# Optimization experiments

Measured on AMD Instinct MI355X. Metric: run time of the kernel, lower is better.

The kernel has to match this reference:

```python
import jax, jax.numpy as jnp
import numpy as np

N_NODES, N_EDGES, F_IN, DIM, N_GRAPHS = 50000, 800000, 128, 256, 256


def setup_inputs() -> dict:
    key = jax.random.key(0)
    ks = jax.random.split(key, 6)
    x = jax.random.normal(ks[0], (N_NODES, F_IN), jnp.float32)
    src = jax.random.randint(ks[1], (N_EDGES,), 0, N_NODES, jnp.int32)
    dst = jax.random.randint(ks[2], (N_EDGES,), 0, N_NODES, jnp.int32)
    node2graph = jnp.sort(jax.random.randint(ks[3], (N_NODES,), 0, N_GRAPHS, jnp.int32))
    W1 = jax.random.normal(ks[4], (F_IN, DIM), jnp.float32) * (1.0 / np.sqrt(F_IN))
    b1 = jnp.zeros((DIM,), jnp.float32)
    W2 = jax.random.normal(ks[5], (DIM, DIM), jnp.float32) * (1.0 / np.sqrt(DIM))
    b2 = jnp.zeros((DIM,), jnp.float32)
    return {"x": x, "W1": W1, "b1": b1, "W2": W2, "b2": b2,
            "src": src, "dst": dst, "node2graph": node2graph}


def reference(x, W1, b1, W2, b2, src, dst, node2graph):
    n = x.shape[0]
    ones = jnp.ones(src.shape[0], x.dtype)
    # DGL GraphConv norm='both': symmetric degree normalization, degrees clamped to >= 1
    out_norm = jnp.maximum(jax.ops.segment_sum(ones, src, num_segments=n), 1.0) ** -0.5
    in_norm = jnp.maximum(jax.ops.segment_sum(ones, dst, num_segments=n), 1.0) ** -0.5

    def gcn_layer(h, W, b):
        msg = (h * out_norm[:, None])[src]                      # [E, d] gather
        agg = jax.ops.segment_sum(msg, dst, num_segments=n)     # [N, d] scatter-add
        return (agg * in_norm[:, None]) @ W + b

    h = jax.nn.relu(gcn_layer(x, W1, b1))   # relu on all but last layer
    h = gcn_layer(h, W2, b2)                # last layer: no activation
    # scale: sqrt(dim) / mean node L2 norm (computed on first forward)
    factor = jnp.sqrt(jnp.asarray(DIM, h.dtype)) / jnp.mean(jnp.linalg.norm(h, axis=1))
    h = h * factor
    # SumPooling: per-graph segment sum
    return jax.ops.segment_sum(h, node2graph, num_segments=N_GRAPHS)
```

## Files before the change

kernel.cpp:

```cpp
#include <hip/hip_runtime.h>

#define NODES 50000
#define EDGES 800000
#define FIN 128
#define DIM 256
#define GRAPHS 256
#define PAD_M 50048
#define PRESCALE_BLOCKS (NODES * FIN / 4 / 256)
#define HBLOCKS 256
#define CHUNK (EDGES / HBLOCKS)
#define HALF_N 25000
#define HALF_W 12500
#define RB 98

typedef short short8 __attribute__((ext_vector_type(8)));
typedef float f32x4 __attribute__((ext_vector_type(4)));

__device__ __forceinline__ float bf2f(uint u) { return __uint_as_float(u << 16); }
__device__ __forceinline__ ushort f2bf(float f) {
    uint b = __float_as_uint(f);
    return (ushort)((b + 0x7FFF + ((b >> 16) & 1)) >> 16);
}

__global__ __launch_bounds__(256) void hist2_kernel(const int* __restrict__ src,
                                                    const int* __restrict__ dst,
                                                    uint* __restrict__ histIn,
                                                    uint* __restrict__ histOut) {
    __shared__ uint cur[HALF_W];
    int b = blockIdx.x & 255, tid = threadIdx.x;
    const int* idx = (blockIdx.x < HBLOCKS) ? dst : src;
    uint* histG    = (blockIdx.x < HBLOCKS) ? histIn : histOut;
    int base = b * CHUNK;
    for (int half = 0; half < 2; ++half) {
        for (int j = tid; j < HALF_W; j += 256) cur[j] = 0;
        __syncthreads();
        int lo = half * HALF_N;
        for (int e = base + tid; e < base + CHUNK; e += 256) {
            int local = idx[e] - lo;
            if ((unsigned)local < (unsigned)HALF_N)
                atomicAdd(&cur[local >> 1], 1u << ((local & 1) * 16));
        }
        __syncthreads();
        uint* dstp = histG + (size_t)b * (2 * HALF_W) + half * HALF_W;
        for (int j = tid; j < HALF_W; j += 256) dstp[j] = cur[j];
        __syncthreads();
    }
}

__global__ __launch_bounds__(256) void reduce_hist_kernel(uint* __restrict__ histIn,
                                                          const uint* __restrict__ histOut,
                                                          int* __restrict__ deg_in,
                                                          float* __restrict__ in_norm,
                                                          float* __restrict__ out_norm,
                                                          int* __restrict__ block_sums) {
    __shared__ int red[4];
    int t32 = blockIdx.x * 256 + threadIdx.x;
    uint lo = 0, hi = 0;
    if (t32 < 2 * HALF_W) {
#pragma unroll 4
        for (int c = 0; c < HBLOCKS; ++c) {
            size_t a = (size_t)c * (2 * HALF_W) + t32;
            uint u = histIn[a];
            histIn[a] = lo | (hi << 16);
            lo += u & 0xFFFFu;
            hi += u >> 16;
        }
        uint olo = 0, ohi = 0;
#pragma unroll 4
        for (int c = 0; c < HBLOCKS; ++c) {
            uint u = histOut[(size_t)c * (2 * HALF_W) + t32];
            olo += u & 0xFFFFu;
            ohi += u >> 16;
        }
        int n0 = 2 * t32;
        deg_in[n0]     = (int)lo;
        deg_in[n0 + 1] = (int)hi;
        in_norm[n0]      = rsqrtf(fmaxf((float)lo, 1.0f));
        in_norm[n0 + 1]  = rsqrtf(fmaxf((float)hi, 1.0f));
        out_norm[n0]     = rsqrtf(fmaxf((float)olo, 1.0f));
        out_norm[n0 + 1] = rsqrtf(fmaxf((float)ohi, 1.0f));
    }
    int s = (int)(lo + hi);
    int wave = threadIdx.x >> 6, lane = threadIdx.x & 63;
#pragma unroll
    for (int off = 32; off > 0; off >>= 1) s += __shfl_down(s, off);
    if (lane == 0) red[wave] = s;
    __syncthreads();
    if (threadIdx.x == 0) block_sums[blockIdx.x] = red[0] + red[1] + red[2] + red[3];
}

__global__ __launch_bounds__(256) void scan_blocksums(int* __restrict__ block_sums,
                                                      int* __restrict__ row_start,
                                                      float* __restrict__ norm_sum, int nb, int n) {
    __shared__ int s[256];
    int t = threadIdx.x;
    if (t == 0) *norm_sum = 0.0f;
    int v = (t < nb) ? block_sums[t] : 0;
    s[t] = v;
    __syncthreads();
#pragma unroll
    for (int off = 1; off < 256; off <<= 1) {
        int u = (t >= off) ? s[t - off] : 0;
        __syncthreads();
        s[t] += u;
        __syncthreads();
    }
    if (t < nb) block_sums[t] = s[t] - v;
    if (t == nb - 1) row_start[n] = s[t];
}

__global__ __launch_bounds__(256) void scanfinal_prep_kernel(const int* __restrict__ deg,
                                                             const int* __restrict__ block_sums,
                                                             int* __restrict__ row_start,
                                                             const float* __restrict__ x,
                                                             const float* __restrict__ out_norm,
                                                             ushort* __restrict__ xs,
                                                             const float* __restrict__ W1,
                                                             ushort* __restrict__ W1T,
                                                             const float* __restrict__ W2,
                                                             ushort* __restrict__ W2T) {
    __shared__ int s[256];
    int b = blockIdx.x, t = threadIdx.x;
    if (b < RB) {
        int i0 = b * 512 + 2 * t;
        int v0 = (i0 < NODES) ? deg[i0] : 0;
        int v1 = (i0 + 1 < NODES) ? deg[i0 + 1] : 0;
        int pair = v0 + v1;
        s[t] = pair;
        __syncthreads();
#pragma unroll
        for (int off = 1; off < 256; off <<= 1) {
            int u = (t >= off) ? s[t - off] : 0;
            __syncthreads();
            s[t] += u;
            __syncthreads();
        }
        int excl = block_sums[b] + s[t] - pair;
        if (i0 < NODES) row_start[i0] = excl;
        if (i0 + 1 < NODES) row_start[i0 + 1] = excl + v0;
    } else if (b < RB + PRESCALE_BLOCKS) {
        int i = (b - RB) * 256 + t;
        int row = i >> 5;
        float on = out_norm[row];
        float4 v = ((const float4*)x)[i];
        ushort4 o;
        o.x = f2bf(v.x * on); o.y = f2bf(v.y * on);
        o.z = f2bf(v.z * on); o.w = f2bf(v.w * on);
        ((ushort4*)xs)[i] = o;
    } else if (b < RB + PRESCALE_BLOCKS + FIN * DIM / 256) {
        int i = (b - RB - PRESCALE_BLOCKS) * 256 + t;
        int n = i >> 7, k = i & 127;
        W1T[i] = f2bf(W1[(size_t)k * DIM + n]);
    } else {
        int i = (b - RB - PRESCALE_BLOCKS - FIN * DIM / 256) * 256 + t;
        int n = i >> 8, k = i & 255;
        W2T[i] = f2bf(W2[(size_t)k * DIM + n]);
    }
}

__global__ __launch_bounds__(256) void scatter_lds_kernel(const int* __restrict__ src,
                                                          const int* __restrict__ dst,
                                                          const uint* __restrict__ histIn,
                                                          const int* __restrict__ row_start,
                                                          int* __restrict__ src_sorted) {
    __shared__ uint cur[HALF_W];
    int b = blockIdx.x, tid = threadIdx.x;
    int base = b * CHUNK;
    for (int half = 0; half < 2; ++half) {
        const uint* offp = histIn + (size_t)b * (2 * HALF_W) + half * HALF_W;
        for (int j = tid; j < HALF_W; j += 256) cur[j] = offp[j];
        __syncthreads();
        int lo = half * HALF_N;
        for (int e = base + tid; e < base + CHUNK; e += 256) {
            int d = dst[e];
            int local = d - lo;
            if ((unsigned)local < (unsigned)HALF_N) {
                int sel = (local & 1) * 16;
                uint old = atomicAdd(&cur[local >> 1], 1u << sel);
                int pos = row_start[d] + (int)((old >> sel) & 0xFFFFu);
                src_sorted[pos] = src[e];
            }
        }
        __syncthreads();
    }
}

template<int D>
__global__ __launch_bounds__(256) void agg_kernel(const ushort* __restrict__ in,
                                                  const int* __restrict__ row_start,
                                                  const int* __restrict__ src_sorted,
                                                  const float* __restrict__ in_norm,
                                                  ushort* __restrict__ out) {
    constexpr int VPL = D / 64;
    constexpr int NU = VPL / 2;
    int wave = threadIdx.x >> 6, lane = threadIdx.x & 63;
    int node = blockIdx.x * 4 + wave;
    if (node >= NODES) return;
    int off = lane * VPL;
    int e0 = row_start[node], e1 = row_start[node + 1];
    float acc[VPL] = {};
    int niter = (e1 - e0 + 7) >> 3;
    for (int it = 0; it < niter; ++it) {
        int eb = e0 + it * 8;
        int idx[8];
#pragma unroll
        for (int j = 0; j < 8; ++j) idx[j] = src_sorted[min(eb + j, e1 - 1)];
        uint u[8][NU];
#pragma unroll
        for (int j = 0; j < 8; ++j) {
            const uint* p = (const uint*)(in + (size_t)idx[j] * D + off);
#pragma unroll
            for (int q = 0; q < NU; ++q) u[j][q] = p[q];
        }
#pragma unroll
        for (int j = 0; j < 8; ++j) {
            uint ok = (eb + j < e1) ? 0xFFFFFFFFu : 0u;
#pragma unroll
            for (int q = 0; q < NU; ++q) {
                uint uu = u[j][q] & ok;
                acc[2*q]   += bf2f(uu & 0xFFFFu);
                acc[2*q+1] += bf2f(uu >> 16);
            }
        }
    }
    float inn = in_norm[node];
    uint* po = (uint*)(out + (size_t)node * D + off);
#pragma unroll
    for (int q = 0; q < NU; ++q) {
        uint lo = f2bf(acc[2*q] * inn);
        uint hi = f2bf(acc[2*q+1] * inn);
        po[q] = lo | (hi << 16);
    }
}

template<int K, int MODE>
__global__ __launch_bounds__(256) void gemm_mfma_kernel(const ushort* __restrict__ A,
                                                        const ushort* __restrict__ WT,
                                                        const float* __restrict__ bias,
                                                        ushort* __restrict__ Cout,
                                                        const float* __restrict__ scale,
                                                        float* __restrict__ norm_sum,
                                                        int M) {
    __shared__ float rowsq[4][64];
    int lane = threadIdx.x & 63, wave = threadIdx.x >> 6;
    int m0 = blockIdx.x * 64, n0 = wave * 64;
    int ll = lane & 15, lh = lane >> 4;
    f32x4 acc[4][4] = {};
    const ushort* Ab = A  + (size_t)(m0 + ll) * K + lh * 8;
    const ushort* Bb = WT + (size_t)(n0 + ll) * K + lh * 8;
#pragma unroll
    for (int k0 = 0; k0 < K; k0 += 32) {
        short8 a[4], b[4];
#pragma unroll
        for (int mi = 0; mi < 4; ++mi) a[mi] = *(const short8*)(Ab + (size_t)mi * 16 * K + k0);
#pragma unroll
        for (int ni = 0; ni < 4; ++ni) b[ni] = *(const short8*)(Bb + (size_t)ni * 16 * K + k0);
#pragma unroll
        for (int mi = 0; mi < 4; ++mi)
#pragma unroll
            for (int ni = 0; ni < 4; ++ni)
                acc[mi][ni] = __builtin_amdgcn_mfma_f32_16x16x32_bf16(a[mi], b[ni], acc[mi][ni], 0, 0, 0);
    }
#pragma unroll
    for (int mi = 0; mi < 4; ++mi) {
#pragma unroll
        for (int r = 0; r < 4; ++r) {
            int row = m0 + mi * 16 + lh * 4 + r;
            float sc = (MODE == 0 && row < M) ? scale[row] : 1.0f;
            float p = 0.0f;
#pragma unroll
            for (int ni = 0; ni < 4; ++ni) {
                int col = n0 + ni * 16 + ll;
                float v = acc[mi][ni][r] + bias[col];
                if (MODE == 0) v = fmaxf(v, 0.0f) * sc;
                else p += v * v;
                if (row < M) Cout[(size_t)row * DIM + col] = f2bf(v);
            }
            if (MODE == 1) {
#pragma unroll
                for (int m = 1; m < 16; m <<= 1) p += __shfl_xor(p, m);
                if (ll == 0) rowsq[wave][mi * 16 + lh * 4 + r] = p;
            }
        }
    }
    if (MODE == 1) {
        __syncthreads();
        if (threadIdx.x < 64) {
            int lr = threadIdx.x;
            float s = rowsq[0][lr] + rowsq[1][lr] + rowsq[2][lr] + rowsq[3][lr];
            float l = (m0 + lr < M) ? sqrtf(s) : 0.0f;
#pragma unroll
            for (int m = 32; m > 0; m >>= 1) l += __shfl_down(l, m);
            if (lr == 0) atomicAdd(norm_sum, l);
        }
    }
}

__global__ __launch_bounds__(256) void pool_kernel(const ushort* __restrict__ h2,
                                                   const int* __restrict__ n2g,
                                                   const float* __restrict__ norm_sum,
                                                   float* __restrict__ out) {
    int g = blockIdx.x, f = threadIdx.x;
    int lo = 0, hi = NODES;
    while (lo < hi) { int mid = (lo + hi) >> 1; if (n2g[mid] < g) lo = mid + 1; else hi = mid; }
    int start = lo;
    hi = NODES;
    while (lo < hi) { int mid = (lo + hi) >> 1; if (n2g[mid] < g + 1) lo = mid + 1; else hi = mid; }
    int end = lo;
    float acc = 0.0f;
    int i = start;
    for (; i + 3 < end; i += 4) {
        acc += (bf2f((uint)h2[(size_t)(i + 0) * DIM + f]) + bf2f((uint)h2[(size_t)(i + 1) * DIM + f]))
             + (bf2f((uint)h2[(size_t)(i + 2) * DIM + f]) + bf2f((uint)h2[(size_t)(i + 3) * DIM + f]));
    }
    for (; i < end; ++i) acc += bf2f((uint)h2[(size_t)i * DIM + f]);
    float factor = 16.0f * (float)NODES / *norm_sum;
    out[(size_t)g * DIM + f] = acc * factor;
}

extern "C" void kernel_launch(void* const* d_in, const int* in_sizes, int n_in,
                              void* d_out, int out_size, void* d_ws, size_t ws_size,
                              hipStream_t stream) {
    const float* x  = (const float*)d_in[0];
    const float* W1 = (const float*)d_in[1];
    const float* b1 = (const float*)d_in[2];
    const float* W2 = (const float*)d_in[3];
    const float* b2 = (const float*)d_in[4];
    const int* src = (const int*)d_in[5];
    const int* dst = (const int*)d_in[6];
    const int* n2g = (const int*)d_in[7];
    float* out = (float*)d_out;

    char* ws = (char*)d_ws;
    size_t off = 0;
    auto alloc = [&](size_t bytes) {
        char* p = ws + off;
        off = (off + bytes + 255) & ~(size_t)255;
        return p;
    };
    uint* histIn    = (uint*)alloc((size_t)HBLOCKS * 2 * HALF_W * 4);
    uint* histOut   = (uint*)alloc((size_t)HBLOCKS * 2 * HALF_W * 4);
    int* deg_in     = (int*)alloc(NODES * 4);
    float* out_norm = (float*)alloc(NODES * 4);
    float* in_norm  = (float*)alloc(NODES * 4);
    int* row_start  = (int*)alloc((NODES + 1) * 4);
    int* src_sorted = (int*)alloc(EDGES * 4);
    int* block_sums = (int*)alloc(RB * 4);
    float* norm_sum = (float*)alloc(4);
    ushort* W1T     = (ushort*)alloc((size_t)DIM * FIN * 2);
    ushort* W2T     = (ushort*)alloc((size_t)DIM * DIM * 2);
    ushort* xs  = (ushort*)alloc((size_t)PAD_M * FIN * 2);
    ushort* A1  = (ushort*)alloc((size_t)PAD_M * FIN * 2);
    ushort* h1s = (ushort*)alloc((size_t)PAD_M * DIM * 2);
    ushort* A2 = xs;
    ushort* h2 = h1s;

    hist2_kernel<<<2 * HBLOCKS, 256, 0, stream>>>(src, dst, histIn, histOut);
    reduce_hist_kernel<<<RB, 256, 0, stream>>>(histIn, histOut, deg_in, in_norm, out_norm, block_sums);
    scan_blocksums<<<1, 256, 0, stream>>>(block_sums, row_start, norm_sum, RB, NODES);
    scanfinal_prep_kernel<<<RB + PRESCALE_BLOCKS + FIN * DIM / 256 + DIM * DIM / 256, 256, 0, stream>>>(
        deg_in, block_sums, row_start, x, out_norm, xs, W1, W1T, W2, W2T);
    scatter_lds_kernel<<<HBLOCKS, 256, 0, stream>>>(src, dst, histIn, row_start, src_sorted);

    agg_kernel<FIN><<<(NODES + 3) / 4, 256, 0, stream>>>(xs, row_start, src_sorted, in_norm, A1);
    gemm_mfma_kernel<FIN, 0><<<PAD_M / 64, 256, 0, stream>>>(A1, W1T, b1, h1s, out_norm, norm_sum, NODES);

    agg_kernel<DIM><<<(NODES + 3) / 4, 256, 0, stream>>>(h1s, row_start, src_sorted, in_norm, A2);
    gemm_mfma_kernel<DIM, 1><<<PAD_M / 64, 256, 0, stream>>>(A2, W2T, b2, h2, nullptr, norm_sum, NODES);

    pool_kernel<<<GRAPHS, 256, 0, stream>>>(h2, n2g, norm_sum, out);
}
```

Baseline: 269.0 us.

## Fuse neighbor aggregation into MFMA GEMM via LDS tile and merge scan kernels

Each GEMM block now gathers and aggregates its own 64 node rows into an LDS tile, then runs the bf16 MFMA GEMM directly from LDS. This removes the intermediate aggregated-matrix write and reread and one kernel launch per layer. The single-block block-sum scan is folded into the scanfinal kernel, where every block redundantly scans the block sums, and the norm_sum zeroing moves into the histogram kernel. The trade-off is parallelism: aggregation now runs with 782 blocks of 16 serial rows per wave instead of 12500 blocks with one node per wave, which can reduce latency hiding for the random gathers.

```diff
diff --git a/kernel.cpp b/kernel.cpp
--- a/kernel.cpp
+++ b/kernel.cpp
@@ -25,8 +25,10 @@
 __global__ __launch_bounds__(256) void hist2_kernel(const int* __restrict__ src,
                                                     const int* __restrict__ dst,
                                                     uint* __restrict__ histIn,
-                                                    uint* __restrict__ histOut) {
+                                                    uint* __restrict__ histOut,
+                                                    float* __restrict__ norm_sum) {
     __shared__ uint cur[HALF_W];
+    if (blockIdx.x == 0 && threadIdx.x == 0) *norm_sum = 0.0f;
     int b = blockIdx.x & 255, tid = threadIdx.x;
     const int* idx = (blockIdx.x < HBLOCKS) ? dst : src;
     uint* histG    = (blockIdx.x < HBLOCKS) ? histIn : histOut;
@@ -89,26 +91,6 @@
     if (threadIdx.x == 0) block_sums[blockIdx.x] = red[0] + red[1] + red[2] + red[3];
 }
 
-__global__ __launch_bounds__(256) void scan_blocksums(int* __restrict__ block_sums,
-                                                      int* __restrict__ row_start,
-                                                      float* __restrict__ norm_sum, int nb, int n) {
-    __shared__ int s[256];
-    int t = threadIdx.x;
-    if (t == 0) *norm_sum = 0.0f;
-    int v = (t < nb) ? block_sums[t] : 0;
-    s[t] = v;
-    __syncthreads();
-#pragma unroll
-    for (int off = 1; off < 256; off <<= 1) {
-        int u = (t >= off) ? s[t - off] : 0;
-        __syncthreads();
-        s[t] += u;
-        __syncthreads();
-    }
-    if (t < nb) block_sums[t] = s[t] - v;
-    if (t == nb - 1) row_start[n] = s[t];
-}
-
 __global__ __launch_bounds__(256) void scanfinal_prep_kernel(const int* __restrict__ deg,
                                                              const int* __restrict__ block_sums,
                                                              int* __restrict__ row_start,
@@ -122,6 +104,18 @@
     __shared__ int s[256];
     int b = blockIdx.x, t = threadIdx.x;
     if (b < RB) {
+        s[t] = (t < RB) ? block_sums[t] : 0;
+        __syncthreads();
+#pragma unroll
+        for (int off = 1; off < 256; off <<= 1) {
+            int u = (t >= off) ? s[t - off] : 0;
+            __syncthreads();
+            s[t] += u;
+            __syncthreads();
+        }
+        int block_off = (b == 0) ? 0 : s[b - 1];
+        if (b == 0 && t == 0) row_start[NODES] = s[RB - 1];
+        __syncthreads();
         int i0 = b * 512 + 2 * t;
         int v0 = (i0 < NODES) ? deg[i0] : 0;
         int v1 = (i0 + 1 < NODES) ? deg[i0 + 1] : 0;
@@ -135,7 +129,7 @@
             s[t] += u;
             __syncthreads();
         }
-        int excl = block_sums[b] + s[t] - pair;
+        int excl = block_off + s[t] - pair;
         if (i0 < NODES) row_start[i0] = excl;
         if (i0 + 1 < NODES) row_start[i0 + 1] = excl + v0;
     } else if (b < RB + PRESCALE_BLOCKS) {
@@ -185,74 +179,73 @@
     }
 }
 
-template<int D>
-__global__ __launch_bounds__(256) void agg_kernel(const ushort* __restrict__ in,
-                                                  const int* __restrict__ row_start,
-                                                  const int* __restrict__ src_sorted,
-                                                  const float* __restrict__ in_norm,
-                                                  ushort* __restrict__ out) {
-    constexpr int VPL = D / 64;
+template<int K, int MODE>
+__global__ __launch_bounds__(256) void gemm_agg_kernel(const ushort* __restrict__ in,
+                                                       const int* __restrict__ row_start,
+                                                       const int* __restrict__ src_sorted,
+                                                       const float* __restrict__ in_norm,
+                                                       const ushort* __restrict__ WT,
+                                                       const float* __restrict__ bias,
+                                                       ushort* __restrict__ Cout,
+                                                       const float* __restrict__ scale,
+                                                       float* __restrict__ norm_sum,
+                                                       int M) {
+    constexpr int LK = K + 8;
+    __shared__ ushort At[64][LK];
+    __shared__ float rowsq[4][64];
+    constexpr int VPL = K / 64;
     constexpr int NU = VPL / 2;
-    int wave = threadIdx.x >> 6, lane = threadIdx.x & 63;
-    int node = blockIdx.x * 4 + wave;
-    if (node >= NODES) return;
+    int lane = threadIdx.x & 63, wave = threadIdx.x >> 6;
+    int m0 = blockIdx.x * 64;
     int off = lane * VPL;
-    int e0 = row_start[node], e1 = row_start[node + 1];
-    float acc[VPL] = {};
-    int niter = (e1 - e0 + 7) >> 3;
-    for (int it = 0; it < niter; ++it) {
-        int eb = e0 + it * 8;
-        int idx[8];
-#pragma unroll
-        for (int j = 0; j < 8; ++j) idx[j] = src_sorted[min(eb + j, e1 - 1)];
-        uint u[8][NU];
-#pragma unroll
-        for (int j = 0; j < 8; ++j) {
-            const uint* p = (const uint*)(in + (size_t)idx[j] * D + off);
-#pragma unroll
-            for (int q = 0; q < NU; ++q) u[j][q] = p[q];
-        }
-#pragma unroll
-        for (int j = 0; j < 8; ++j) {
-            uint ok = (eb + j < e1) ? 0xFFFFFFFFu : 0u;
-#pragma unroll
-            for (int q = 0; q < NU; ++q) {
-                uint uu = u[j][q] & ok;
-                acc[2*q]   += bf2f(uu & 0xFFFFu);
-                acc[2*q+1] += bf2f(uu >> 16);
+    for (int r = 0; r < 16; ++r) {
+        int node = m0 + wave * 16 + r;
+        float acc[VPL] = {};
+        if (node < NODES) {
+            int e0 = row_start[node], e1 = row_start[node + 1];
+            int niter = (e1 - e0 + 7) >> 3;
+            for (int it = 0; it < niter; ++it) {
+                int eb = e0 + it * 8;
+                int idx[8];
+#pragma unroll
+                for (int j = 0; j < 8; ++j) idx[j] = src_sorted[min(eb + j, e1 - 1)];
+                uint u[8][NU];
+#pragma unroll
+                for (int j = 0; j < 8; ++j) {
+                    const uint* p = (const uint*)(in + (size_t)idx[j] * K + off);
+#pragma unroll
+                    for (int q = 0; q < NU; ++q) u[j][q] = p[q];
+                }
+#pragma unroll
+                for (int j = 0; j < 8; ++j) {
+                    uint ok = (eb + j < e1) ? 0xFFFFFFFFu : 0u;
+#pragma unroll
+                    for (int q = 0; q < NU; ++q) {
+                        uint uu = u[j][q] & ok;
+                        acc[2*q]   += bf2f(uu & 0xFFFFu);
+                        acc[2*q+1] += bf2f(uu >> 16);
+                    }
+                }
             }
-        }
-    }
-    float inn = in_norm[node];
-    uint* po = (uint*)(out + (size_t)node * D + off);
-#pragma unroll
-    for (int q = 0; q < NU; ++q) {
-        uint lo = f2bf(acc[2*q] * inn);
-        uint hi = f2bf(acc[2*q+1] * inn);
-        po[q] = lo | (hi << 16);
-    }
-}
-
-template<int K, int MODE>
-__global__ __launch_bounds__(256) void gemm_mfma_kernel(const ushort* __restrict__ A,
-                                                        const ushort* __restrict__ WT,
-                                                        const float* __restrict__ bias,
-                                                        ushort* __restrict__ Cout,
-                                                        const float* __restrict__ scale,
-                                                        float* __restrict__ norm_sum,
-                                                        int M) {
-    __shared__ float rowsq[4][64];
-    int lane = threadIdx.x & 63, wave = threadIdx.x >> 6;
-    int m0 = blockIdx.x * 64, n0 = wave * 64;
+            float inn = in_norm[node];
+#pragma unroll
+            for (int v = 0; v < VPL; ++v) acc[v] *= inn;
+        }
+        uint* po = (uint*)&At[wave * 16 + r][off];
+#pragma unroll
+        for (int q = 0; q < NU; ++q)
+            po[q] = (uint)f2bf(acc[2*q]) | ((uint)f2bf(acc[2*q+1]) << 16);
+    }
+    __syncthreads();
+    int n0 = wave * 64;
     int ll = lane & 15, lh = lane >> 4;
     f32x4 acc[4][4] = {};
-    const ushort* Ab = A  + (size_t)(m0 + ll) * K + lh * 8;
     const ushort* Bb = WT + (size_t)(n0 + ll) * K + lh * 8;
 #pragma unroll
     for (int k0 = 0; k0 < K; k0 += 32) {
         short8 a[4], b[4];
 #pragma unroll
-        for (int mi = 0; mi < 4; ++mi) a[mi] = *(const short8*)(Ab + (size_t)mi * 16 * K + k0);
+        for (int mi = 0; mi < 4; ++mi) a[mi] = *(const short8*)&At[mi * 16 + ll][k0 + lh * 8];
 #pragma unroll
         for (int ni = 0; ni < 4; ++ni) b[ni] = *(const short8*)(Bb + (size_t)ni * 16 * K + k0);
 #pragma unroll
@@ -349,24 +342,21 @@
     float* norm_sum = (float*)alloc(4);
     ushort* W1T     = (ushort*)alloc((size_t)DIM * FIN * 2);
     ushort* W2T     = (ushort*)alloc((size_t)DIM * DIM * 2);
-    ushort* xs  = (ushort*)alloc((size_t)PAD_M * FIN * 2);
-    ushort* A1  = (ushort*)alloc((size_t)PAD_M * FIN * 2);
-    ushort* h1s = (ushort*)alloc((size_t)PAD_M * DIM * 2);
-    ushort* A2 = xs;
-    ushort* h2 = h1s;
-
-    hist2_kernel<<<2 * HBLOCKS, 256, 0, stream>>>(src, dst, histIn, histOut);
+    ushort* xs      = (ushort*)alloc((size_t)NODES * FIN * 2);
+    ushort* h1s     = (ushort*)alloc((size_t)PAD_M * DIM * 2);
+    ushort* h2      = (ushort*)alloc((size_t)PAD_M * DIM * 2);
+
+    hist2_kernel<<<2 * HBLOCKS, 256, 0, stream>>>(src, dst, histIn, histOut, norm_sum);
     reduce_hist_kernel<<<RB, 256, 0, stream>>>(histIn, histOut, deg_in, in_norm, out_norm, block_sums);
-    scan_blocksums<<<1, 256, 0, stream>>>(block_sums, row_start, norm_sum, RB, NODES);
     scanfinal_prep_kernel<<<RB + PRESCALE_BLOCKS + FIN * DIM / 256 + DIM * DIM / 256, 256, 0, stream>>>(
         deg_in, block_sums, row_start, x, out_norm, xs, W1, W1T, W2, W2T);
     scatter_lds_kernel<<<HBLOCKS, 256, 0, stream>>>(src, dst, histIn, row_start, src_sorted);
 
-    agg_kernel<FIN><<<(NODES + 3) / 4, 256, 0, stream>>>(xs, row_start, src_sorted, in_norm, A1);
-    gemm_mfma_kernel<FIN, 0><<<PAD_M / 64, 256, 0, stream>>>(A1, W1T, b1, h1s, out_norm, norm_sum, NODES);
-
-    agg_kernel<DIM><<<(NODES + 3) / 4, 256, 0, stream>>>(h1s, row_start, src_sorted, in_norm, A2);
-    gemm_mfma_kernel<DIM, 1><<<PAD_M / 64, 256, 0, stream>>>(A2, W2T, b2, h2, nullptr, norm_sum, NODES);
+    gemm_agg_kernel<FIN, 0><<<PAD_M / 64, 256, 0, stream>>>(
+        xs, row_start, src_sorted, in_norm, W1T, b1, h1s, out_norm, norm_sum, NODES);
+
+    gemm_agg_kernel<DIM, 1><<<PAD_M / 64, 256, 0, stream>>>(
+        h1s, row_start, src_sorted, in_norm, W2T, b2, h2, nullptr, norm_sum, NODES);
 
     pool_kernel<<<GRAPHS, 256, 0, stream>>>(h2, n2g, norm_sum, out);
 }
```

After: 327.1 us. +21.6%, slower.

## Fold block-sum scan into per-block scan and merge scatter with prep kernel

Applied to the files above, without the earlier changes.

Removes the single-block scan_blocksums launch: each scanfinal block now redundantly scans the 98 block sums itself to get its offset. The x prescale and weight transpose/bf16 conversion move out of the scan kernel into the scatter kernel as extra blocks, so they overlap with the LDS-atomic scatter. norm_sum zeroing moves into hist2. This saves one launch and one serialized dependency step, at the cost of redundant scan work per block and larger LDS use by the prep blocks in the merged kernel.

```diff
diff --git a/kernel.cpp b/kernel.cpp
--- a/kernel.cpp
+++ b/kernel.cpp
@@ -25,8 +25,10 @@
 __global__ __launch_bounds__(256) void hist2_kernel(const int* __restrict__ src,
                                                     const int* __restrict__ dst,
                                                     uint* __restrict__ histIn,
-                                                    uint* __restrict__ histOut) {
+                                                    uint* __restrict__ histOut,
+                                                    float* __restrict__ norm_sum) {
     __shared__ uint cur[HALF_W];
+    if (blockIdx.x == 0 && threadIdx.x == 0) *norm_sum = 0.0f;
     int b = blockIdx.x & 255, tid = threadIdx.x;
     const int* idx = (blockIdx.x < HBLOCKS) ? dst : src;
     uint* histG    = (blockIdx.x < HBLOCKS) ? histIn : histOut;
@@ -89,14 +91,12 @@
     if (threadIdx.x == 0) block_sums[blockIdx.x] = red[0] + red[1] + red[2] + red[3];
 }
 
-__global__ __launch_bounds__(256) void scan_blocksums(int* __restrict__ block_sums,
-                                                      int* __restrict__ row_start,
-                                                      float* __restrict__ norm_sum, int nb, int n) {
+__global__ __launch_bounds__(256) void scanfinal_kernel(const int* __restrict__ deg,
+                                                        const int* __restrict__ block_sums,
+                                                        int* __restrict__ row_start) {
     __shared__ int s[256];
-    int t = threadIdx.x;
-    if (t == 0) *norm_sum = 0.0f;
-    int v = (t < nb) ? block_sums[t] : 0;
-    s[t] = v;
+    int b = blockIdx.x, t = threadIdx.x;
+    s[t] = (t < RB) ? block_sums[t] : 0;
     __syncthreads();
 #pragma unroll
     for (int off = 1; off < 256; off <<= 1) {
@@ -105,83 +105,81 @@
         s[t] += u;
         __syncthreads();
     }
-    if (t < nb) block_sums[t] = s[t] - v;
-    if (t == nb - 1) row_start[n] = s[t];
-}
-
-__global__ __launch_bounds__(256) void scanfinal_prep_kernel(const int* __restrict__ deg,
-                                                             const int* __restrict__ block_sums,
-                                                             int* __restrict__ row_start,
-                                                             const float* __restrict__ x,
-                                                             const float* __restrict__ out_norm,
-                                                             ushort* __restrict__ xs,
-                                                             const float* __restrict__ W1,
-                                                             ushort* __restrict__ W1T,
-                                                             const float* __restrict__ W2,
-                                                             ushort* __restrict__ W2T) {
-    __shared__ int s[256];
-    int b = blockIdx.x, t = threadIdx.x;
-    if (b < RB) {
-        int i0 = b * 512 + 2 * t;
-        int v0 = (i0 < NODES) ? deg[i0] : 0;
-        int v1 = (i0 + 1 < NODES) ? deg[i0 + 1] : 0;
-        int pair = v0 + v1;
-        s[t] = pair;
-        __syncthreads();
-#pragma unroll
-        for (int off = 1; off < 256; off <<= 1) {
-            int u = (t >= off) ? s[t - off] : 0;
+    int block_off = (b == 0) ? 0 : s[b - 1];
+    if (b == 0 && t == 0) row_start[NODES] = s[RB - 1];
+    __syncthreads();
+    int i0 = b * 512 + 2 * t;
+    int v0 = (i0 < NODES) ? deg[i0] : 0;
+    int v1 = (i0 + 1 < NODES) ? deg[i0 + 1] : 0;
+    int pair = v0 + v1;
+    s[t] = pair;
+    __syncthreads();
+#pragma unroll
+    for (int off = 1; off < 256; off <<= 1) {
+        int u = (t >= off) ? s[t - off] : 0;
+        __syncthreads();
+        s[t] += u;
+        __syncthreads();
+    }
+    int excl = block_off + s[t] - pair;
+    if (i0 < NODES) row_start[i0] = excl;
+    if (i0 + 1 < NODES) row_start[i0 + 1] = excl + v0;
+}
+
+__global__ __launch_bounds__(256) void scatter_prep_kernel(const int* __restrict__ src,
+                                                           const int* __restrict__ dst,
+                                                           const uint* __restrict__ histIn,
+                                                           const int* __restrict__ row_start,
+                                                           int* __restrict__ src_sorted,
+                                                           const float* __restrict__ x,
+                                                           const float* __restrict__ out_norm,
+                                                           ushort* __restrict__ xs,
+                                                           const float* __restrict__ W1,
+                                                           ushort* __restrict__ W1T,
+                                                           const float* __restrict__ W2,
+                                                           ushort* __restrict__ W2T) {
+    __shared__ uint cur[HALF_W];
+    int tid = threadIdx.x;
+    if (blockIdx.x < HBLOCKS) {
+        int b = blockIdx.x;
+        int base = b * CHUNK;
+        for (int half = 0; half < 2; ++half) {
+            const uint* offp = histIn + (size_t)b * (2 * HALF_W) + half * HALF_W;
+            for (int j = tid; j < HALF_W; j += 256) cur[j] = offp[j];
             __syncthreads();
-            s[t] += u;
+            int lo = half * HALF_N;
+            for (int e = base + tid; e < base + CHUNK; e += 256) {
+                int d = dst[e];
+                int local = d - lo;
+                if ((unsigned)local < (unsigned)HALF_N) {
+                    int sel = (local & 1) * 16;
+                    uint old = atomicAdd(&cur[local >> 1], 1u << sel);
+                    int pos = row_start[d] + (int)((old >> sel) & 0xFFFFu);
+                    src_sorted[pos] = src[e];
+                }
+            }
             __syncthreads();
         }
-        int excl = block_sums[b] + s[t] - pair;
-        if (i0 < NODES) row_start[i0] = excl;
-        if (i0 + 1 < NODES) row_start[i0 + 1] = excl + v0;
-    } else if (b < RB + PRESCALE_BLOCKS) {
-        int i = (b - RB) * 256 + t;
-        int row = i >> 5;
-        float on = out_norm[row];
-        float4 v = ((const float4*)x)[i];
-        ushort4 o;
-        o.x = f2bf(v.x * on); o.y = f2bf(v.y * on);
-        o.z = f2bf(v.z * on); o.w = f2bf(v.w * on);
-        ((ushort4*)xs)[i] = o;
-    } else if (b < RB + PRESCALE_BLOCKS + FIN * DIM / 256) {
-        int i = (b - RB - PRESCALE_BLOCKS) * 256 + t;
-        int n = i >> 7, k = i & 127;
-        W1T[i] = f2bf(W1[(size_t)k * DIM + n]);
     } else {
-        int i = (b - RB - PRESCALE_BLOCKS - FIN * DIM / 256) * 256 + t;
-        int n = i >> 8, k = i & 255;
-        W2T[i] = f2bf(W2[(size_t)k * DIM + n]);
-    }
-}
-
-__global__ __launch_bounds__(256) void scatter_lds_kernel(const int* __restrict__ src,
-                                                          const int* __restrict__ dst,
-                                                          const uint* __restrict__ histIn,
-                                                          const int* __restrict__ row_start,
-                                                          int* __restrict__ src_sorted) {
-    __shared__ uint cur[HALF_W];
-    int b = blockIdx.x, tid = threadIdx.x;
-    int base = b * CHUNK;
-    for (int half = 0; half < 2; ++half) {
-        const uint* offp = histIn + (size_t)b * (2 * HALF_W) + half * HALF_W;
-        for (int j = tid; j < HALF_W; j += 256) cur[j] = offp[j];
-        __syncthreads();
-        int lo = half * HALF_N;
-        for (int e = base + tid; e < base + CHUNK; e += 256) {
-            int d = dst[e];
-            int local = d - lo;
-            if ((unsigned)local < (unsigned)HALF_N) {
-                int sel = (local & 1) * 16;
-                uint old = atomicAdd(&cur[local >> 1], 1u << sel);
-                int pos = row_start[d] + (int)((old >> sel) & 0xFFFFu);
-                src_sorted[pos] = src[e];
-            }
-        }
-        __syncthreads();
+        int bb = blockIdx.x - HBLOCKS;
+        if (bb < PRESCALE_BLOCKS) {
+            int i = bb * 256 + tid;
+            int row = i >> 5;
+            float on = out_norm[row];
+            float4 v = ((const float4*)x)[i];
+            ushort4 o;
+            o.x = f2bf(v.x * on); o.y = f2bf(v.y * on);
+            o.z = f2bf(v.z * on); o.w = f2bf(v.w * on);
+            ((ushort4*)xs)[i] = o;
+        } else if (bb < PRESCALE_BLOCKS + FIN * DIM / 256) {
+            int i = (bb - PRESCALE_BLOCKS) * 256 + tid;
+            int n = i >> 7, k = i & 127;
+            W1T[i] = f2bf(W1[(size_t)k * DIM + n]);
+        } else {
+            int i = (bb - PRESCALE_BLOCKS - FIN * DIM / 256) * 256 + tid;
+            int n = i >> 8, k = i & 255;
+            W2T[i] = f2bf(W2[(size_t)k * DIM + n]);
+        }
     }
 }
 
@@ -355,12 +353,11 @@
     ushort* A2 = xs;
     ushort* h2 = h1s;
 
-    hist2_kernel<<<2 * HBLOCKS, 256, 0, stream>>>(src, dst, histIn, histOut);
+    hist2_kernel<<<2 * HBLOCKS, 256, 0, stream>>>(src, dst, histIn, histOut, norm_sum);
     reduce_hist_kernel<<<RB, 256, 0, stream>>>(histIn, histOut, deg_in, in_norm, out_norm, block_sums);
-    scan_blocksums<<<1, 256, 0, stream>>>(block_sums, row_start, norm_sum, RB, NODES);
-    scanfinal_prep_kernel<<<RB + PRESCALE_BLOCKS + FIN * DIM / 256 + DIM * DIM / 256, 256, 0, stream>>>(
-        deg_in, block_sums, row_start, x, out_norm, xs, W1, W1T, W2, W2T);
-    scatter_lds_kernel<<<HBLOCKS, 256, 0, stream>>>(src, dst, histIn, row_start, src_sorted);
+    scanfinal_kernel<<<RB, 256, 0, stream>>>(deg_in, block_sums, row_start);
+    scatter_prep_kernel<<<HBLOCKS + PRESCALE_BLOCKS + FIN * DIM / 256 + DIM * DIM / 256, 256, 0, stream>>>(
+        src, dst, histIn, row_start, src_sorted, x, out_norm, xs, W1, W1T, W2, W2T);
 
     agg_kernel<FIN><<<(NODES + 3) / 4, 256, 0, stream>>>(xs, row_start, src_sorted, in_norm, A1);
     gemm_mfma_kernel<FIN, 0><<<PAD_M / 64, 256, 0, stream>>>(A1, W1T, b1, h1s, out_norm, norm_sum, NODES);
```

Result: no change. 265.3 us (-1.4%).
